# Optimization experiments

Measured on AMD Instinct MI355X. Metric: run time of the kernel, lower is better.

## Reference

```python
import jax, jax.numpy as jnp
import numpy as np

NUM_HEADS = 16


def setup_inputs() -> dict:
    key = jax.random.key(0)
    k0, k1, k2, k3 = jax.random.split(key, 4)
    S, dim = 8192, 1280              # packed vision tokens, embed dim
    H = NUM_HEADS
    D = dim // H                      # head_dim = 80
    n_seg = 8                         # 8 images x 1024 patches
    L = S // n_seg
    return {
        "hidden_states": jax.random.normal(k0, (S, dim), jnp.float32),
        "rotary_pos_emb": jax.random.normal(k1, (S, D // 2), jnp.float32),
        "w_qkv": jax.random.normal(k2, (3 * dim, dim), jnp.float32) * 0.02,
        "b_qkv": jnp.zeros((3 * dim,), jnp.float32),
        "w_proj": jax.random.normal(k3, (dim, dim), jnp.float32) * 0.02,
        "b_proj": jnp.zeros((dim,), jnp.float32),
        "cu_seqlens": jnp.arange(n_seg + 1, dtype=jnp.int32) * L,
    }


def _rotate_half(x):
    x1, x2 = jnp.split(x, 2, axis=-1)
    return jnp.concatenate([-x2, x1], axis=-1)


def _apply_rope(t, freqs):
    # t: [S, H, D]; freqs: [S, D//2]. Matches cat+rotate_half formulation
    # (cos/sin repeated to full head_dim), computed in float32.
    emb = jnp.concatenate([freqs, freqs], axis=-1)          # [S, D]
    cos = jnp.cos(emb)[:, None, :]                          # [S, 1, D]
    sin = jnp.sin(emb)[:, None, :]
    return t * cos + _rotate_half(t) * sin


def reference(hidden_states, rotary_pos_emb, w_qkv, b_qkv, w_proj, b_proj, cu_seqlens):
    S, dim = hidden_states.shape
    H = NUM_HEADS
    D = dim // H
    n_seg = cu_seqlens.shape[0] - 1   # equal-length packed segments
    L = S // n_seg

    qkv = hidden_states @ w_qkv.T + b_qkv                   # [S, 3*dim]
    q, k, v = jnp.split(qkv, 3, axis=-1)
    q = q.reshape(S, H, D)
    k = k.reshape(S, H, D)
    v = v.reshape(S, H, D)

    q = _apply_rope(q, rotary_pos_emb)
    k = _apply_rope(k, rotary_pos_emb)

    # block-diagonal varlen attention: batch over segments instead of an
    # [S, S] dense mask (honors the cu_seqlens sparsity structure)
    qs = q.reshape(n_seg, L, H, D)
    ks = k.reshape(n_seg, L, H, D)
    vs = v.reshape(n_seg, L, H, D)
    scale = D ** -0.5
    scores = jnp.einsum('blhd,bthd->bhlt', qs, ks) * scale  # [n_seg, H, L, L]
    probs = jax.nn.softmax(scores, axis=-1)
    ctx = jnp.einsum('bhlt,bthd->blhd', probs, vs)          # [n_seg, L, H, D]
    ctx = ctx.reshape(S, dim)

    return ctx @ w_proj.T + b_proj                          # [S, dim]
```

## Files before the change

kernel.cpp:

```cpp
#include <hip/hip_runtime.h>
#include <hip/hip_bf16.h>
#include <math.h>

#define S_TOK   8192
#define DIM     1280
#define NHEAD   16
#define HDIM    80
#define NSEG    8
#define SEGLEN  1024
#define QKV_LD  3840
#define DPAD    96

typedef __attribute__((ext_vector_type(8)))  short bf16x8;
typedef __attribute__((ext_vector_type(4)))  float f32x4;
typedef __attribute__((ext_vector_type(16))) float f32x16;

__device__ __forceinline__ short f2b(float x) {
  __hip_bfloat16 h = __float2bfloat16(x);
  return *reinterpret_cast<short*>(&h);
}
__device__ __forceinline__ float b2f(short x) {
  __hip_bfloat16 h;
  *reinterpret_cast<short*>(&h) = x;
  return __bfloat162float(h);
}

__device__ __forceinline__ void gl_lds16(const void* g, void* l) {
  __builtin_amdgcn_global_load_lds(
      (const __attribute__((address_space(1))) unsigned int*)g,
      (__attribute__((address_space(3))) unsigned int*)l, 16, 0, 0);
}

__global__ __launch_bounds__(256) void cast_f32_bf16(
    const float* __restrict__ in, short* __restrict__ out, int n4)
{
  const int i = blockIdx.x * 256 + threadIdx.x;
  if (i >= n4) return;
  const float4 v = ((const float4*)in)[i];
  short4 o;
  o.x = f2b(v.x); o.y = f2b(v.y); o.z = f2b(v.z); o.w = f2b(v.w);
  ((short4*)out)[i] = o;
}

template<bool OUT_BF16>
__global__ __launch_bounds__(256) void gemm_mfma_nt(
    const short* __restrict__ A, const short* __restrict__ B,
    const float* __restrict__ bias, void* __restrict__ Cout,
    int M, int N, int K)
{
  __shared__ short As[128 * 32];
  __shared__ short Bs[128 * 32];
  const int t = threadIdx.x;
  const int wave = t >> 6, lane = t & 63;
  const int q = lane >> 4, r = lane & 15;
  const int bm = blockIdx.y * 128, bn = blockIdx.x * 128;
  const int wr = (wave >> 1) * 64, wc = (wave & 1) * 64;

  f32x4 acc[4][4];
#pragma unroll
  for (int i = 0; i < 4; ++i)
#pragma unroll
    for (int j = 0; j < 4; ++j) acc[i][j] = (f32x4)(0.f);

  for (int k0 = 0; k0 < K; k0 += 32) {
    __syncthreads();
#pragma unroll
    for (int i = 0; i < 2; ++i) {
      const int c = i * 256 + t;
      const int row = c >> 2, off = (c & 3) * 8;
      gl_lds16(A + (size_t)(bm + row) * K + k0 + off, As + c * 8);
      gl_lds16(B + (size_t)(bn + row) * K + k0 + off, Bs + c * 8);
    }
    __syncthreads();

    bf16x8 af[4], bg[4];
#pragma unroll
    for (int mt = 0; mt < 4; ++mt)
      af[mt] = *(const bf16x8*)&As[(wr + mt * 16 + r) * 32 + q * 8];
#pragma unroll
    for (int nt = 0; nt < 4; ++nt)
      bg[nt] = *(const bf16x8*)&Bs[(wc + nt * 16 + r) * 32 + q * 8];
#pragma unroll
    for (int mt = 0; mt < 4; ++mt)
#pragma unroll
      for (int nt = 0; nt < 4; ++nt)
        acc[mt][nt] = __builtin_amdgcn_mfma_f32_16x16x32_bf16(
            af[mt], bg[nt], acc[mt][nt], 0, 0, 0);
  }

#pragma unroll
  for (int mt = 0; mt < 4; ++mt)
#pragma unroll
    for (int nt = 0; nt < 4; ++nt)
#pragma unroll
      for (int reg = 0; reg < 4; ++reg) {
        const int mrow = bm + wr + mt * 16 + q * 4 + reg;
        const int ncol = bn + wc + nt * 16 + r;
        const float v = acc[mt][nt][reg] + bias[ncol];
        if (OUT_BF16)
          ((short*)Cout)[(size_t)mrow * N + ncol] = f2b(v);
        else
          ((float*)Cout)[(size_t)mrow * N + ncol] = v;
      }
}

__global__ __launch_bounds__(256) void rope_cast(
    const short* __restrict__ qkvb, const float* __restrict__ rot,
    short* __restrict__ Qb, short* __restrict__ Kb)
{
  const int idx = blockIdx.x * 256 + threadIdx.x;
  const int j = idx % 48;
  const int h = (idx / 48) % NHEAD;
  const int s = idx / (48 * NHEAD);
  short* qo = Qb + ((size_t)s * NHEAD + h) * DPAD;
  short* ko = Kb + ((size_t)s * NHEAD + h) * DPAD;
  if (j < 40) {
    const float f = rot[s * 40 + j];
    const float c = cosf(f), sn = sinf(f);
    const short* qi = qkvb + (size_t)s * QKV_LD + h * HDIM;
    const short* ki = qi + DIM;
    const float scale = 0.11180339887498949f * 1.4426950408889634f;
    const float q0 = b2f(qi[j]), q1 = b2f(qi[j + 40]);
    qo[j]      = f2b((q0 * c - q1 * sn) * scale);
    qo[j + 40] = f2b((q1 * c + q0 * sn) * scale);
    const float k0 = b2f(ki[j]), k1 = b2f(ki[j + 40]);
    ko[j]      = f2b(k0 * c - k1 * sn);
    ko[j + 40] = f2b(k1 * c + k0 * sn);
  } else {
    const int z = 80 + (j - 40);
    qo[z] = 0; qo[z + 8] = 0;
    ko[z] = 0; ko[z + 8] = 0;
  }
}

__global__ __launch_bounds__(256) void v_transpose(
    const short* __restrict__ qkvb, short* __restrict__ Vt)
{
  const int tid = blockIdx.x * 256 + threadIdx.x;
  const int c   = tid >> 13;
  const int kv  = tid & 8191;
  const int head = c / 10;
  const int d0   = (c % 10) * 8;
  const int seg  = kv >> 10;
  const bf16x8 v = *(const bf16x8*)(qkvb + (size_t)kv * QKV_LD + 2 * DIM +
                                    head * HDIM + d0);
  short* ob = Vt + ((size_t)(seg * NHEAD + head) * HDIM + d0) * SEGLEN + (kv & 1023);
#pragma unroll
  for (int j = 0; j < 8; ++j)
    ob[(size_t)j * SEGLEN] = v[j];
}

#define LQK 104
#define LVT 72
#define NTILE 16

__global__ __launch_bounds__(256, 2) void attn_mfma(
    const short* __restrict__ Qb, const short* __restrict__ Kb,
    const short* __restrict__ Vtg, short* __restrict__ ctxb)
{
  __shared__ short Ks[64 * LQK];
  __shared__ short Vs[96 * LVT];

  const int t = threadIdx.x;
  const int wave = t >> 6, lane = t & 63;
  const int c = lane & 31, hi = lane >> 5;
  const int seg = blockIdx.z, head = blockIdx.y;
  const int m0 = blockIdx.x * 256;
  const size_t srow0 = (size_t)seg * SEGLEN;
  const size_t vbase = (size_t)(seg * NHEAD + head) * HDIM * SEGLEN;

  for (int i = t; i < 16 * LVT / 2; i += 256)
    ((int*)(Vs + 80 * LVT))[i] = 0;

  bf16x8 qf[2][6];
#pragma unroll
  for (int u = 0; u < 2; ++u)
#pragma unroll
    for (int ks = 0; ks < 6; ++ks)
      qf[u][ks] = *(const bf16x8*)(
          Qb + ((srow0 + m0 + wave * 64 + u * 32 + c) * NHEAD + head) * DPAD +
          ks * 16 + hi * 8);

  f32x16 o[3][2];
#pragma unroll
  for (int d = 0; d < 3; ++d)
#pragma unroll
    for (int u = 0; u < 2; ++u) o[d][u] = (f32x16)(0.f);
  float m_[2] = {-1e30f, -1e30f}, l_[2] = {0.f, 0.f};

  const int kc_row[3] = {(0 * 256 + t) / 12, (1 * 256 + t) / 12, (2 * 256 + t) / 12};
  const int kc_off[3] = {((0 * 256 + t) % 12) * 8, ((1 * 256 + t) % 12) * 8,
                         ((2 * 256 + t) % 12) * 8};
  bf16x8 kreg[3], vreg[3];

#define LOAD_K(n0)                                                             \
  {                                                                            \
    _Pragma("unroll")                                                          \
    for (int i = 0; i < 3; ++i)                                                \
      kreg[i] = *(const bf16x8*)(                                              \
          Kb + ((srow0 + (n0) + kc_row[i]) * NHEAD + head) * DPAD + kc_off[i]);\
  }
#define LOAD_V(n0)                                                             \
  {                                                                            \
    _Pragma("unroll")                                                          \
    for (int i = 0; i < 3; ++i) {                                              \
      const int cc = i * 256 + t;                                              \
      if (cc < 640)                                                            \
        vreg[i] = *(const bf16x8*)(Vtg + vbase + (size_t)(cc >> 3) * SEGLEN +  \
                                   (n0) + (cc & 7) * 8);                       \
    }                                                                          \
  }

  LOAD_K(0)
  LOAD_V(0)

  for (int tile = 0; tile < NTILE; ++tile) {
    __syncthreads();
#pragma unroll
    for (int i = 0; i < 3; ++i)
      *(bf16x8*)&Ks[kc_row[i] * LQK + kc_off[i]] = kreg[i];
#pragma unroll
    for (int i = 0; i < 3; ++i) {
      const int cc = i * 256 + t;
      if (cc < 640)
        *(bf16x8*)&Vs[(cc >> 3) * LVT + (cc & 7) * 8] = vreg[i];
    }
    __syncthreads();

    if (tile + 1 < NTILE) LOAD_K((tile + 1) * 64)

    f32x16 s[2][2];
#pragma unroll
    for (int tt = 0; tt < 2; ++tt)
#pragma unroll
      for (int u = 0; u < 2; ++u) s[tt][u] = (f32x16)(0.f);
    __builtin_amdgcn_s_setprio(1);
#pragma unroll
    for (int tt = 0; tt < 2; ++tt)
#pragma unroll
      for (int ks = 0; ks < 6; ++ks) {
        const bf16x8 kf =
            *(const bf16x8*)&Ks[(tt * 32 + c) * LQK + ks * 16 + hi * 8];
        s[tt][0] = __builtin_amdgcn_mfma_f32_32x32x16_bf16(kf, qf[0][ks], s[tt][0], 0, 0, 0);
        s[tt][1] = __builtin_amdgcn_mfma_f32_32x32x16_bf16(kf, qf[1][ks], s[tt][1], 0, 0, 0);
      }
    __builtin_amdgcn_s_setprio(0);

    bf16x8 pf[2][4];
#pragma unroll
    for (int u = 0; u < 2; ++u) {
      float a0 = -1e30f, a1 = -1e30f, a2 = -1e30f, a3 = -1e30f;
#pragma unroll
      for (int tt = 0; tt < 2; ++tt)
#pragma unroll
        for (int i = 0; i < 16; i += 4) {
          a0 = fmaxf(a0, s[tt][u][i]);
          a1 = fmaxf(a1, s[tt][u][i + 1]);
          a2 = fmaxf(a2, s[tt][u][i + 2]);
          a3 = fmaxf(a3, s[tt][u][i + 3]);
        }
      float mx = fmaxf(fmaxf(a0, a1), fmaxf(a2, a3));
      mx = fmaxf(mx, __shfl_xor(mx, 32));
      if (!__all(mx <= m_[u])) {
        const float mn = fmaxf(m_[u], mx);
        const float corr = exp2f(m_[u] - mn);
        m_[u] = mn;
        l_[u] *= corr;
#pragma unroll
        for (int d = 0; d < 3; ++d)
#pragma unroll
          for (int i = 0; i < 16; ++i) o[d][u][i] *= corr;
      }
      float s0 = 0.f, s1 = 0.f, s2 = 0.f, s3 = 0.f;
#pragma unroll
      for (int tt = 0; tt < 2; ++tt)
#pragma unroll
        for (int i = 0; i < 16; i += 4) {
          const float e0 = exp2f(s[tt][u][i] - m_[u]);
          const float e1 = exp2f(s[tt][u][i + 1] - m_[u]);
          const float e2 = exp2f(s[tt][u][i + 2] - m_[u]);
          const float e3 = exp2f(s[tt][u][i + 3] - m_[u]);
          s[tt][u][i] = e0; s[tt][u][i + 1] = e1;
          s[tt][u][i + 2] = e2; s[tt][u][i + 3] = e3;
          s0 += e0; s1 += e1; s2 += e2; s3 += e3;
        }
      float sum = (s0 + s1) + (s2 + s3);
      sum += __shfl_xor(sum, 32);
      l_[u] += sum;

      unsigned d8[2][8];
#pragma unroll
      for (int tt = 0; tt < 2; ++tt)
#pragma unroll
        for (int i = 0; i < 8; ++i)
          d8[tt][i] = ((unsigned)(unsigned short)f2b(s[tt][u][2 * i + 1]) << 16) |
                      (unsigned short)f2b(s[tt][u][2 * i]);
      unsigned rcv[2][8 / 2];
#pragma unroll
      for (int tt = 0; tt < 2; ++tt) {
        const unsigned sd0 = hi ? d8[tt][0] : d8[tt][2];
        const unsigned sd1 = hi ? d8[tt][1] : d8[tt][3];
        const unsigned sd2 = hi ? d8[tt][4] : d8[tt][6];
        const unsigned sd3 = hi ? d8[tt][5] : d8[tt][7];
        rcv[tt][0] = __shfl_xor((int)sd0, 32);
        rcv[tt][1] = __shfl_xor((int)sd1, 32);
        rcv[tt][2] = __shfl_xor((int)sd2, 32);
        rcv[tt][3] = __shfl_xor((int)sd3, 32);
      }
#pragma unroll
      for (int ks = 0; ks < 4; ++ks) {
        const int tt = ks >> 1, k2 = ks & 1;
        int4 pw;
        pw.x = hi ? (int)rcv[tt][2 * k2]     : (int)d8[tt][4 * k2];
        pw.y = hi ? (int)rcv[tt][2 * k2 + 1] : (int)d8[tt][4 * k2 + 1];
        pw.z = hi ? (int)d8[tt][4 * k2 + 2]  : (int)rcv[tt][2 * k2];
        pw.w = hi ? (int)d8[tt][4 * k2 + 3]  : (int)rcv[tt][2 * k2 + 1];
        pf[u][ks] = *reinterpret_cast<bf16x8*>(&pw);
      }
    }

    if (tile + 1 < NTILE) LOAD_V((tile + 1) * 64)

    __builtin_amdgcn_s_setprio(1);
#pragma unroll
    for (int dt = 0; dt < 3; ++dt)
#pragma unroll
      for (int ks = 0; ks < 4; ++ks) {
        const bf16x8 vf =
            *(const bf16x8*)&Vs[(dt * 32 + c) * LVT + ks * 16 + hi * 8];
        o[dt][0] = __builtin_amdgcn_mfma_f32_32x32x16_bf16(vf, pf[0][ks], o[dt][0], 0, 0, 0);
        o[dt][1] = __builtin_amdgcn_mfma_f32_32x32x16_bf16(vf, pf[1][ks], o[dt][1], 0, 0, 0);
      }
    __builtin_amdgcn_s_setprio(0);
  }

#pragma unroll
  for (int u = 0; u < 2; ++u) {
    const float inv = 1.f / l_[u];
    const size_t row = srow0 + m0 + wave * 64 + u * 32 + c;
#pragma unroll
    for (int dt = 0; dt < 3; ++dt)
#pragma unroll
      for (int g = 0; g < 4; ++g) {
        const int d0 = dt * 32 + 8 * g + 4 * hi;
        if (d0 < HDIM) {
          short4 v4;
          v4.x = f2b(o[dt][u][4 * g + 0] * inv);
          v4.y = f2b(o[dt][u][4 * g + 1] * inv);
          v4.z = f2b(o[dt][u][4 * g + 2] * inv);
          v4.w = f2b(o[dt][u][4 * g + 3] * inv);
          *(short4*)&ctxb[row * DIM + head * HDIM + d0] = v4;
        }
      }
  }
}

extern "C" void kernel_launch(void* const* d_in, const int* in_sizes, int n_in,
                              void* d_out, int out_size, void* d_ws, size_t ws_size,
                              hipStream_t stream)
{
  const float* hs    = (const float*)d_in[0];
  const float* rot   = (const float*)d_in[1];
  const float* wqkv  = (const float*)d_in[2];
  const float* bqkv  = (const float*)d_in[3];
  const float* wproj = (const float*)d_in[4];
  const float* bproj = (const float*)d_in[5];
  float* out = (float*)d_out;

  char* w = (char*)d_ws;
  short* hs_b    = (short*)w;  w += (size_t)S_TOK * DIM * 2;
  short* wqkv_b  = (short*)w;  w += (size_t)QKV_LD * DIM * 2;
  short* wproj_b = (short*)w;  w += (size_t)DIM * DIM * 2;
  short* qkv_b   = (short*)w;  w += (size_t)S_TOK * QKV_LD * 2;
  short* Qb      = (short*)w;  w += (size_t)S_TOK * NHEAD * DPAD * 2;
  short* Kb      = (short*)w;  w += (size_t)S_TOK * NHEAD * DPAD * 2;
  short* ctx_b   = (short*)w;  w += (size_t)S_TOK * DIM * 2;
  short* Vt_g    = hs_b;

  dim3 blk(256);

  cast_f32_bf16<<<dim3(S_TOK * DIM / 4 / 256), blk, 0, stream>>>(hs, hs_b, S_TOK * DIM / 4);
  cast_f32_bf16<<<dim3(QKV_LD * DIM / 4 / 256), blk, 0, stream>>>(wqkv, wqkv_b, QKV_LD * DIM / 4);
  cast_f32_bf16<<<dim3(DIM * DIM / 4 / 256), blk, 0, stream>>>(wproj, wproj_b, DIM * DIM / 4);

  gemm_mfma_nt<true><<<dim3(QKV_LD / 128, S_TOK / 128), blk, 0, stream>>>(
      hs_b, wqkv_b, bqkv, qkv_b, S_TOK, QKV_LD, DIM);

  rope_cast<<<dim3(S_TOK * NHEAD * 48 / 256), blk, 0, stream>>>(qkv_b, rot, Qb, Kb);

  v_transpose<<<dim3(160 * S_TOK / 256), blk, 0, stream>>>(qkv_b, Vt_g);

  attn_mfma<<<dim3(SEGLEN / 256, NHEAD, NSEG), blk, 0, stream>>>(Qb, Kb, Vt_g, ctx_b);

  gemm_mfma_nt<false><<<dim3(DIM / 128, S_TOK / 128), blk, 0, stream>>>(
      ctx_b, wproj_b, bproj, out, S_TOK, DIM, DIM);
}
```

Measured before the change: 459.0 us.

## Double-buffer attention K/V tiles and widen GEMM K-step with swizzled LDS

In attention, K and V tiles now live in two LDS buffers so the next tile is stored while the current one is consumed, with register prefetch two tiles ahead. This removes one barrier per iteration and lets global loads overlap compute. The GEMM K-step goes from 32 to 64 with an XOR-swizzled LDS layout, halving barrier count and reducing bank conflicts. LDS use doubles in both kernels, which may lower occupancy, and attention holds more live registers.

```diff
diff --git a/kernel.cpp b/kernel.cpp
--- a/kernel.cpp
+++ b/kernel.cpp
@@ -48,8 +48,8 @@
     const float* __restrict__ bias, void* __restrict__ Cout,
     int M, int N, int K)
 {
-  __shared__ short As[128 * 32];
-  __shared__ short Bs[128 * 32];
+  __shared__ short As[128 * 64];
+  __shared__ short Bs[128 * 64];
   const int t = threadIdx.x;
   const int wave = t >> 6, lane = t & 63;
   const int q = lane >> 4, r = lane & 15;
@@ -62,30 +62,38 @@
 #pragma unroll
     for (int j = 0; j < 4; ++j) acc[i][j] = (f32x4)(0.f);
 
-  for (int k0 = 0; k0 < K; k0 += 32) {
+  for (int k0 = 0; k0 < K; k0 += 64) {
     __syncthreads();
 #pragma unroll
-    for (int i = 0; i < 2; ++i) {
+    for (int i = 0; i < 4; ++i) {
       const int c = i * 256 + t;
-      const int row = c >> 2, off = (c & 3) * 8;
-      gl_lds16(A + (size_t)(bm + row) * K + k0 + off, As + c * 8);
-      gl_lds16(B + (size_t)(bn + row) * K + k0 + off, Bs + c * 8);
+      const int row = c >> 3, slot = c & 7;
+      const int soff = (slot ^ (row & 7)) * 8;
+      gl_lds16(A + (size_t)(bm + row) * K + k0 + soff, As + c * 8);
+      gl_lds16(B + (size_t)(bn + row) * K + k0 + soff, Bs + c * 8);
     }
     __syncthreads();
 
-    bf16x8 af[4], bg[4];
-#pragma unroll
-    for (int mt = 0; mt < 4; ++mt)
-      af[mt] = *(const bf16x8*)&As[(wr + mt * 16 + r) * 32 + q * 8];
-#pragma unroll
-    for (int nt = 0; nt < 4; ++nt)
-      bg[nt] = *(const bf16x8*)&Bs[(wc + nt * 16 + r) * 32 + q * 8];
-#pragma unroll
-    for (int mt = 0; mt < 4; ++mt)
-#pragma unroll
-      for (int nt = 0; nt < 4; ++nt)
-        acc[mt][nt] = __builtin_amdgcn_mfma_f32_16x16x32_bf16(
-            af[mt], bg[nt], acc[mt][nt], 0, 0, 0);
+#pragma unroll
+    for (int kk = 0; kk < 2; ++kk) {
+      bf16x8 af[4], bg[4];
+#pragma unroll
+      for (int mt = 0; mt < 4; ++mt) {
+        const int row = wr + mt * 16 + r;
+        af[mt] = *(const bf16x8*)&As[row * 64 + ((kk * 4 + q) ^ (row & 7)) * 8];
+      }
+#pragma unroll
+      for (int nt = 0; nt < 4; ++nt) {
+        const int row = wc + nt * 16 + r;
+        bg[nt] = *(const bf16x8*)&Bs[row * 64 + ((kk * 4 + q) ^ (row & 7)) * 8];
+      }
+#pragma unroll
+      for (int mt = 0; mt < 4; ++mt)
+#pragma unroll
+        for (int nt = 0; nt < 4; ++nt)
+          acc[mt][nt] = __builtin_amdgcn_mfma_f32_16x16x32_bf16(
+              af[mt], bg[nt], acc[mt][nt], 0, 0, 0);
+    }
   }
 
 #pragma unroll
@@ -158,8 +166,8 @@
     const short* __restrict__ Qb, const short* __restrict__ Kb,
     const short* __restrict__ Vtg, short* __restrict__ ctxb)
 {
-  __shared__ short Ks[64 * LQK];
-  __shared__ short Vs[96 * LVT];
+  __shared__ short Ks[2][64 * LQK];
+  __shared__ short Vs[2][96 * LVT];
 
   const int t = threadIdx.x;
   const int wave = t >> 6, lane = t & 63;
@@ -169,8 +177,10 @@
   const size_t srow0 = (size_t)seg * SEGLEN;
   const size_t vbase = (size_t)(seg * NHEAD + head) * HDIM * SEGLEN;
 
-  for (int i = t; i < 16 * LVT / 2; i += 256)
-    ((int*)(Vs + 80 * LVT))[i] = 0;
+  for (int i = t; i < 16 * LVT / 2; i += 256) {
+    ((int*)(Vs[0] + 80 * LVT))[i] = 0;
+    ((int*)(Vs[1] + 80 * LVT))[i] = 0;
+  }
 
   bf16x8 qf[2][6];
 #pragma unroll
@@ -210,24 +220,32 @@
                                    (n0) + (cc & 7) * 8);                       \
     }                                                                          \
   }
+#define STORE_KV(buf)                                                          \
+  {                                                                            \
+    _Pragma("unroll")                                                          \
+    for (int i = 0; i < 3; ++i)                                                \
+      *(bf16x8*)&Ks[buf][kc_row[i] * LQK + kc_off[i]] = kreg[i];               \
+    _Pragma("unroll")                                                          \
+    for (int i = 0; i < 3; ++i) {                                              \
+      const int cc = i * 256 + t;                                              \
+      if (cc < 640)                                                            \
+        *(bf16x8*)&Vs[buf][(cc >> 3) * LVT + (cc & 7) * 8] = vreg[i];          \
+    }                                                                          \
+  }
 
   LOAD_K(0)
   LOAD_V(0)
+  STORE_KV(0)
+  LOAD_K(64)
+  LOAD_V(64)
 
   for (int tile = 0; tile < NTILE; ++tile) {
     __syncthreads();
-#pragma unroll
-    for (int i = 0; i < 3; ++i)
-      *(bf16x8*)&Ks[kc_row[i] * LQK + kc_off[i]] = kreg[i];
-#pragma unroll
-    for (int i = 0; i < 3; ++i) {
-      const int cc = i * 256 + t;
-      if (cc < 640)
-        *(bf16x8*)&Vs[(cc >> 3) * LVT + (cc & 7) * 8] = vreg[i];
-    }
-    __syncthreads();
-
-    if (tile + 1 < NTILE) LOAD_K((tile + 1) * 64)
+    const int cur = tile & 1;
+    if (tile + 1 < NTILE) STORE_KV(cur ^ 1)
+    if (tile + 2 < NTILE) { LOAD_K((tile + 2) * 64) LOAD_V((tile + 2) * 64) }
+    const short* ksc = Ks[cur];
+    const short* vsc = Vs[cur];
 
     f32x16 s[2][2];
 #pragma unroll
@@ -240,7 +258,7 @@
 #pragma unroll
       for (int ks = 0; ks < 6; ++ks) {
         const bf16x8 kf =
-            *(const bf16x8*)&Ks[(tt * 32 + c) * LQK + ks * 16 + hi * 8];
+            *(const bf16x8*)&ksc[(tt * 32 + c) * LQK + ks * 16 + hi * 8];
         s[tt][0] = __builtin_amdgcn_mfma_f32_32x32x16_bf16(kf, qf[0][ks], s[tt][0], 0, 0, 0);
         s[tt][1] = __builtin_amdgcn_mfma_f32_32x32x16_bf16(kf, qf[1][ks], s[tt][1], 0, 0, 0);
       }
@@ -295,7 +313,7 @@
         for (int i = 0; i < 8; ++i)
           d8[tt][i] = ((unsigned)(unsigned short)f2b(s[tt][u][2 * i + 1]) << 16) |
                       (unsigned short)f2b(s[tt][u][2 * i]);
-      unsigned rcv[2][8 / 2];
+      unsigned rcv[2][4];
 #pragma unroll
       for (int tt = 0; tt < 2; ++tt) {
         const unsigned sd0 = hi ? d8[tt][0] : d8[tt][2];
@@ -319,15 +337,13 @@
       }
     }
 
-    if (tile + 1 < NTILE) LOAD_V((tile + 1) * 64)
-
     __builtin_amdgcn_s_setprio(1);
 #pragma unroll
     for (int dt = 0; dt < 3; ++dt)
 #pragma unroll
       for (int ks = 0; ks < 4; ++ks) {
         const bf16x8 vf =
-            *(const bf16x8*)&Vs[(dt * 32 + c) * LVT + ks * 16 + hi * 8];
+            *(const bf16x8*)&vsc[(dt * 32 + c) * LVT + ks * 16 + hi * 8];
         o[dt][0] = __builtin_amdgcn_mfma_f32_32x32x16_bf16(vf, pf[0][ks], o[dt][0], 0, 0, 0);
         o[dt][1] = __builtin_amdgcn_mfma_f32_32x32x16_bf16(vf, pf[1][ks], o[dt][1], 0, 0, 0);
       }
```

After: 469.3 us. +2.2%, slower.
